# Optimization experiments

Measured on AMD Instinct MI355X. Metric: run time of the kernel, lower is better.

Reference implementation:

```python
import jax, jax.numpy as jnp
import numpy as np


def _logmvv(a, b, c, NT):
    """Log-space batched matrix-vector-vector product (SparseKernelHmmLm.logmvv).

    a: (N, T, C)     log potentials per sparse state
    b: (N, T, C, D)  log left features
    c: (N, T, C, D)  log right features
    Returns (N, T, D, D): out[n,t,i,j] = logsumexp_c(a[n,t,c] + b[n,t,c,i] + c[n,t,c,j])
    Tokens are flattened and zero-padded to NT rows, as in the original kernel.
    """
    N, T, C = a.shape
    D = b.shape[-1]
    nt = N * T
    pad = NT - nt
    af = jnp.concatenate([a.reshape(nt, C), jnp.zeros((pad, C), a.dtype)], 0)          # (NT, C)
    bf = jnp.concatenate([b.reshape(nt, C, D), jnp.zeros((pad, C, D), b.dtype)], 0)    # (NT, C, D)
    cf = jnp.concatenate([c.reshape(nt, C, D), jnp.zeros((pad, C, D), c.dtype)], 0)    # (NT, C, D)

    ab = af[:, :, None] + bf                      # (NT, C, D) log(a*b)
    m1 = jnp.max(ab, axis=1)                      # (NT, D) stabilizer for left factor
    m2 = jnp.max(cf, axis=1)                      # (NT, D) stabilizer for right factor
    e1 = jnp.exp(ab - m1[:, None, :])             # (NT, C, D)
    e2 = jnp.exp(cf - m2[:, None, :])             # (NT, C, D)
    # contraction over sparse states C -> (NT, D, D)
    s = jnp.einsum('nci,ncj->nij', e1, e2)
    out = jnp.log(s) + m1[:, :, None] + m2[:, None, :]
    return out[:nt].reshape(N, T, D, D)


def setup_inputs() -> dict:
    key = jax.random.key(0)
    k1, k2, k3 = jax.random.split(key, 3)
    N, T, C, D = 8, 250, 128, 64
    a = jax.random.normal(k1, (N, T, C), dtype=jnp.float32)
    b = jax.random.normal(k2, (N, T, C, D), dtype=jnp.float32)
    c = jax.random.normal(k3, (N, T, C, D), dtype=jnp.float32)
    return {"a": a, "b": b, "c": c, "NT": 2048}


def reference(a, b, c, NT):
    return _logmvv(a, b, c, NT)
```

## Files before the change

### kernel.cpp

```cpp
#include <hip/hip_runtime.h>
#include <stdint.h>

typedef __attribute__((ext_vector_type(8))) short short8;
typedef __attribute__((ext_vector_type(4))) float f32x4;

#define CDIM 128
#define DDIM 64

__device__ __forceinline__ uint32_t pack2_bf16(float a, float b) {
  uint32_t ua = __float_as_uint(a);
  uint32_t ub = __float_as_uint(b);
  ua = (ua + 0x7FFFu + ((ua >> 16) & 1u)) >> 16;
  ub = (ub + 0x7FFFu + ((ub >> 16) & 1u)) >> 16;
  return ua | (ub << 16);
}

__global__ __launch_bounds__(256, 4) void logmvv_kernel(
    const float* __restrict__ a, const float* __restrict__ b,
    const float* __restrict__ c, float* __restrict__ out) {
  __shared__ __align__(16) uint16_t e2T[DDIM * CDIM];

  const int row = blockIdx.x;
  const int t = threadIdx.x;
  const int lane = t & 63;
  const int w = t >> 6;
  const int l15 = lane & 15;
  const int lq = lane >> 4;
  const int swz = (lane & 7) << 4;

  const float* ap = a + (size_t)row * CDIM;
  const float* bp = b + (size_t)row * (CDIM * DDIM);
  const float* cp = c + (size_t)row * (CDIM * DDIM);

  float cv[32];
#pragma unroll
  for (int p = 0; p < 32; ++p) cv[p] = cp[(w * 32 + p) * DDIM + lane];

  const int colA = 16 * w + l15;
  float bvv[4][8];
#pragma unroll
  for (int kk = 0; kk < 4; ++kk)
#pragma unroll
    for (int e = 0; e < 8; ++e)
      bvv[kk][e] = bp[(kk * 32 + lq * 8 + e) * DDIM + colA];
  float av[4][8];
#pragma unroll
  for (int kk = 0; kk < 4; ++kk) {
    const float4 a0 = *(const float4*)(ap + kk * 32 + lq * 8);
    const float4 a1 = *(const float4*)(ap + kk * 32 + lq * 8 + 4);
    av[kk][0] = a0.x; av[kk][1] = a0.y; av[kk][2] = a0.z; av[kk][3] = a0.w;
    av[kk][4] = a1.x; av[kk][5] = a1.y; av[kk][6] = a1.z; av[kk][7] = a1.w;
  }

  char* e2b = (char*)e2T;
#pragma unroll
  for (int k = 0; k < 4; ++k) {
    const uint32_t r0 = pack2_bf16(__expf(cv[k * 8 + 0]), __expf(cv[k * 8 + 1]));
    const uint32_t r1 = pack2_bf16(__expf(cv[k * 8 + 2]), __expf(cv[k * 8 + 3]));
    const uint32_t r2 = pack2_bf16(__expf(cv[k * 8 + 4]), __expf(cv[k * 8 + 5]));
    const uint32_t r3 = pack2_bf16(__expf(cv[k * 8 + 6]), __expf(cv[k * 8 + 7]));
    *(uint4*)(e2b + lane * 256 + ((w * 64 + k * 16) ^ swz)) =
        make_uint4(r0, r1, r2, r3);
  }

  short8 afrag[4];
#pragma unroll
  for (int kk = 0; kk < 4; ++kk) {
    union { uint32_t u[4]; short8 s; } fr;
#pragma unroll
    for (int p = 0; p < 4; ++p)
      fr.u[p] = pack2_bf16(__expf(av[kk][2 * p] + bvv[kk][2 * p]),
                           __expf(av[kk][2 * p + 1] + bvv[kk][2 * p + 1]));
    afrag[kk] = fr.s;
  }
  asm volatile("" ::"v"(afrag[0]), "v"(afrag[1]), "v"(afrag[2]), "v"(afrag[3]));

  __syncthreads();

  f32x4 acc[4];
#pragma unroll
  for (int tj = 0; tj < 4; ++tj) acc[tj] = (f32x4){0.f, 0.f, 0.f, 0.f};

#pragma unroll
  for (int kk = 0; kk < 4; ++kk) {
    const int cb = kk * 64 + lq * 16;
#pragma unroll
    for (int tj = 0; tj < 4; ++tj) {
      const short8 bf =
          *(const short8*)(e2b + (16 * tj + l15) * 256 + (cb ^ swz));
      acc[tj] =
          __builtin_amdgcn_mfma_f32_16x16x32_bf16(afrag[kk], bf, acc[tj], 0, 0, 0);
    }
  }

  float* op = out + (size_t)row * (DDIM * DDIM);
#pragma unroll
  for (int tj = 0; tj < 4; ++tj)
#pragma unroll
    for (int rr = 0; rr < 4; ++rr)
      op[(16 * w + lq * 4 + rr) * DDIM + 16 * tj + l15] = __logf(acc[tj][rr]);
}

extern "C" void kernel_launch(void* const* d_in, const int* in_sizes, int n_in,
                              void* d_out, int out_size, void* d_ws, size_t ws_size,
                              hipStream_t stream) {
  const float* a = (const float*)d_in[0];
  const float* b = (const float*)d_in[1];
  const float* c = (const float*)d_in[2];
  float* out = (float*)d_out;
  const int nt = in_sizes[0] / CDIM;
  logmvv_kernel<<<nt, 256, 0, stream>>>(a, b, c, out);
}
```

Before: 29.28 us.

## Stage c tile into LDS via direct global-to-LDS loads, reorder exp work

Loads each row's fp32 c tile straight into shared memory with global_load_lds instead of holding it in 32 registers per thread. The b/a exponentials for the A fragments are computed while those async loads are in flight. A barrier is added, then the c values are read back from LDS to build the bf16 transposed tile. The extra 32KB of LDS per block forces occupancy down from 4 to 3 blocks per CU and adds a barrier plus an LDS round trip.

```diff
diff --git a/kernel.cpp b/kernel.cpp
--- a/kernel.cpp
+++ b/kernel.cpp
@@ -15,9 +15,10 @@
   return ua | (ub << 16);
 }
 
-__global__ __launch_bounds__(256, 4) void logmvv_kernel(
+__global__ __launch_bounds__(256, 3) void logmvv_kernel(
     const float* __restrict__ a, const float* __restrict__ b,
     const float* __restrict__ c, float* __restrict__ out) {
+  __shared__ __align__(16) float ldsC[CDIM * DDIM];
   __shared__ __align__(16) uint16_t e2T[DDIM * CDIM];
 
   const int row = blockIdx.x;
@@ -32,49 +33,63 @@
   const float* bp = b + (size_t)row * (CDIM * DDIM);
   const float* cp = c + (size_t)row * (CDIM * DDIM);
 
-  float cv[32];
 #pragma unroll
-  for (int p = 0; p < 32; ++p) cv[p] = cp[(w * 32 + p) * DDIM + lane];
+  for (int i = 0; i < 8; ++i) {
+    const int idx = w * 8 + i;
+    __builtin_amdgcn_global_load_lds(
+        (const __attribute__((address_space(1))) void*)(cp + idx * 256 + lane * 4),
+        (__attribute__((address_space(3))) void*)((char*)ldsC + idx * 1024),
+        16, 0, 0);
+  }
 
   const int colA = 16 * w + l15;
-  float bvv[4][8];
+  float bv[32];
 #pragma unroll
   for (int kk = 0; kk < 4; ++kk)
 #pragma unroll
     for (int e = 0; e < 8; ++e)
-      bvv[kk][e] = bp[(kk * 32 + lq * 8 + e) * DDIM + colA];
-  float av[4][8];
+      bv[kk * 8 + e] = bp[(kk * 32 + lq * 8 + e) * DDIM + colA];
+  asm volatile(""
+               : "+v"(bv[0]), "+v"(bv[1]), "+v"(bv[2]), "+v"(bv[3]),
+                 "+v"(bv[4]), "+v"(bv[5]), "+v"(bv[6]), "+v"(bv[7]),
+                 "+v"(bv[8]), "+v"(bv[9]), "+v"(bv[10]), "+v"(bv[11]),
+                 "+v"(bv[12]), "+v"(bv[13]), "+v"(bv[14]), "+v"(bv[15]),
+                 "+v"(bv[16]), "+v"(bv[17]), "+v"(bv[18]), "+v"(bv[19]),
+                 "+v"(bv[20]), "+v"(bv[21]), "+v"(bv[22]), "+v"(bv[23]),
+                 "+v"(bv[24]), "+v"(bv[25]), "+v"(bv[26]), "+v"(bv[27]),
+                 "+v"(bv[28]), "+v"(bv[29]), "+v"(bv[30]), "+v"(bv[31]));
+
+  short8 afrag[4];
 #pragma unroll
   for (int kk = 0; kk < 4; ++kk) {
     const float4 a0 = *(const float4*)(ap + kk * 32 + lq * 8);
     const float4 a1 = *(const float4*)(ap + kk * 32 + lq * 8 + 4);
-    av[kk][0] = a0.x; av[kk][1] = a0.y; av[kk][2] = a0.z; av[kk][3] = a0.w;
-    av[kk][4] = a1.x; av[kk][5] = a1.y; av[kk][6] = a1.z; av[kk][7] = a1.w;
+    const float aa[8] = {a0.x, a0.y, a0.z, a0.w, a1.x, a1.y, a1.z, a1.w};
+    union { uint32_t u[4]; short8 s; } fr;
+#pragma unroll
+    for (int p = 0; p < 4; ++p)
+      fr.u[p] = pack2_bf16(__expf(aa[2 * p] + bv[kk * 8 + 2 * p]),
+                           __expf(aa[2 * p + 1] + bv[kk * 8 + 2 * p + 1]));
+    afrag[kk] = fr.s;
   }
+  asm volatile("" ::"v"(afrag[0]), "v"(afrag[1]), "v"(afrag[2]), "v"(afrag[3]));
+
+  __syncthreads();
 
   char* e2b = (char*)e2T;
 #pragma unroll
   for (int k = 0; k < 4; ++k) {
-    const uint32_t r0 = pack2_bf16(__expf(cv[k * 8 + 0]), __expf(cv[k * 8 + 1]));
-    const uint32_t r1 = pack2_bf16(__expf(cv[k * 8 + 2]), __expf(cv[k * 8 + 3]));
-    const uint32_t r2 = pack2_bf16(__expf(cv[k * 8 + 4]), __expf(cv[k * 8 + 5]));
-    const uint32_t r3 = pack2_bf16(__expf(cv[k * 8 + 6]), __expf(cv[k * 8 + 7]));
+    float cvv[8];
+#pragma unroll
+    for (int p = 0; p < 8; ++p)
+      cvv[p] = ldsC[(w * 32 + k * 8 + p) * DDIM + lane];
+    const uint32_t r0 = pack2_bf16(__expf(cvv[0]), __expf(cvv[1]));
+    const uint32_t r1 = pack2_bf16(__expf(cvv[2]), __expf(cvv[3]));
+    const uint32_t r2 = pack2_bf16(__expf(cvv[4]), __expf(cvv[5]));
+    const uint32_t r3 = pack2_bf16(__expf(cvv[6]), __expf(cvv[7]));
     *(uint4*)(e2b + lane * 256 + ((w * 64 + k * 16) ^ swz)) =
         make_uint4(r0, r1, r2, r3);
   }
-
-  short8 afrag[4];
-#pragma unroll
-  for (int kk = 0; kk < 4; ++kk) {
-    union { uint32_t u[4]; short8 s; } fr;
-#pragma unroll
-    for (int p = 0; p < 4; ++p)
-      fr.u[p] = pack2_bf16(__expf(av[kk][2 * p] + bvv[kk][2 * p]),
-                           __expf(av[kk][2 * p + 1] + bvv[kk][2 * p + 1]));
-    afrag[kk] = fr.s;
-  }
-  asm volatile("" ::"v"(afrag[0]), "v"(afrag[1]), "v"(afrag[2]), "v"(afrag[3]));
-
   __syncthreads();
 
   f32x4 acc[4];
```

After: 31.37 us. +7.1%, slower.
